# Kernel optimization log

Measured on AMD Instinct MI355X. Metric: run time of the kernel, lower is better.

## Reference

```python
import jax, jax.numpy as jnp
import numpy as np

# Grid config (matches init_kwargs): xbound/ybound [-50,50,0.5], zbound [-10,10,20]
NX = (200, 200, 1)                       # voxels per axis
DX = jnp.array([0.5, 0.5, 20.0], jnp.float32)      # voxel size
LO = jnp.array([-50.0, -50.0, -10.0], jnp.float32)  # grid lower corner (= bx - dx/2)
EXTENT = jnp.array([100.0, 100.0, 20.0], jnp.float32)

B, N, C, D, H, W = 2, 6, 64, 41, 32, 88


def setup_inputs() -> dict:
    key = jax.random.key(0)
    k1, k2, k3 = jax.random.split(key, 3)
    feat = jax.random.normal(k1, (B, N, C, H, W), jnp.float32)
    depth_logits = jax.random.normal(k2, (B, N, D, H, W), jnp.float32)
    geom = jax.random.uniform(k3, (B, N, D, H, W, 3), jnp.float32)  # normalized frustum->ego coords
    return {"feat": feat, "depth_logits": depth_logits, "geom": geom}


def reference(feat, depth_logits, geom):
    # --- Lift: depth-probability-weighted outer product ---
    depth = jax.nn.softmax(depth_logits, axis=2)               # [B,N,D,H,W]
    volume = jnp.einsum('bndhw,bnchw->bndhwc', depth, feat)    # [B,N,D,H,W,C]
    pts = volume.reshape(-1, C)                                # [P, C], P = B*N*D*H*W

    # --- Geometry -> voxel indices (frustum points in ego frame) ---
    world = geom * EXTENT + LO                                 # map [0,1]^3 to grid extent
    vox = jnp.floor((world - LO) / DX).astype(jnp.int32)       # [B,N,D,H,W,3]
    vox = vox.reshape(-1, 3)
    ix, iy, iz = vox[:, 0], vox[:, 1], vox[:, 2]

    nx0, nx1, nx2 = NX
    valid = ((ix >= 0) & (ix < nx0) & (iy >= 0) & (iy < nx1)
             & (iz >= 0) & (iz < nx2))                          # [P]

    pts_per_batch = N * D * H * W
    batch_ix = jnp.repeat(jnp.arange(B, dtype=jnp.int32), pts_per_batch)

    n_vox = nx0 * nx1 * nx2
    seg = ((batch_ix * nx0 + ix) * nx1 + iy) * nx2 + iz
    seg = jnp.where(valid, seg, B * n_vox)                     # invalid -> dummy bucket

    # --- Splat: per-voxel sum (== QuickCumsum sorted-cumsum-diff) ---
    pooled = jax.ops.segment_sum(pts, seg, num_segments=B * n_vox + 1)
    pooled = pooled[:-1].reshape(B, nx0, nx1, nx2, C)          # drop dummy

    # [B, C, Z, X, Y] then collapse Z (=1) into channels -> BEV [B, C, X, Y]
    bev = jnp.transpose(pooled, (0, 4, 3, 1, 2)).reshape(B, C * nx2, nx0, nx1)
    return bev
```

## Files before the change

### kernel.cpp

```cpp
#include <hip/hip_runtime.h>
#include <math.h>
#include <stdint.h>

namespace {
constexpr int kB = 2, kN = 6, kC = 64, kD = 41, kH = 32, kW = 88;
constexpr int kHW = kH * kW;
constexpr int kBN = kB * kN;
constexpr int kNX = 200;
constexpr int kVox = kNX * kNX;
constexpr int kPts = kBN * kD * kHW;
constexpr int kRows4 = kB * kNX * 4;
constexpr int kCap4 = 1120;
constexpr int kOvfCap = 4096;

constexpr int kTiles = kBN * (kHW / 64);
constexpr int kFusedBlks = kTiles * 2;
}

#define FP_BARRIER(x) asm volatile("" : "+v"(x))

__device__ __forceinline__ uint32_t f2bf_rne(float f) {
  uint32_t u = __float_as_uint(f);
  return (u + 0x7FFFu + ((u >> 16) & 1u)) >> 16;
}

__global__ void __launch_bounds__(256) lss_zero(unsigned* __restrict__ cnt) {
  for (int i = threadIdx.x; i <= kRows4; i += 256) cnt[i] = 0u;
}

__global__ void __launch_bounds__(512) lss_fused(
    const float* __restrict__ feat, uint32_t* __restrict__ featT,
    const float* __restrict__ logits, const float* __restrict__ geom,
    unsigned* __restrict__ cnt, uint2* __restrict__ list,
    unsigned* __restrict__ ovf_cnt, uint4* __restrict__ ovf) {
  int blk = blockIdx.x;
  int tid = threadIdx.x;
  if (blk < kTiles) {
    __shared__ float t[64][65];
    int bn = blk / 44, hw0 = (blk % 44) * 64;
    const float* src = feat + (size_t)bn * kC * kHW;
    for (int idx = tid; idx < 64 * 64; idx += 512) {
      int c = idx >> 6, hw = idx & 63;
      t[hw][c] = src[(size_t)c * kHW + hw0 + hw];
    }
    __syncthreads();
    uint32_t* dst = featT + ((size_t)bn * kHW + hw0) * 32;
    for (int idx = tid; idx < 64 * 32; idx += 512) {
      int hw = idx >> 5, j = idx & 31;
      uint32_t lo = f2bf_rne(t[hw][2 * j]);
      uint32_t hi = f2bf_rne(t[hw][2 * j + 1]);
      dst[(size_t)hw * 32 + j] = lo | (hi << 16);
    }
  } else {
    __shared__ unsigned shist[kRows4];
    __shared__ unsigned sbase[kRows4];
    __shared__ float smax[8 * 64];
    __shared__ float ssum[8 * 64];
    int tb = blk - kTiles;
    int bn = tb / 44, hw0 = (tb % 44) * 64;
    int hwl = tid & 63, dg = tid >> 6;
    int hw = hw0 + hwl;
    int b = (bn >= kN) ? 1 : 0;
    int col = bn * kHW + hw;
    int d0 = (dg * kD) >> 3, d1 = ((dg + 1) * kD) >> 3;
    for (int r = tid; r < kRows4; r += 512) shist[r] = 0;
    float x[6];
    float m = -INFINITY;
#pragma unroll
    for (int k = 0; k < 6; ++k) {
      int d = d0 + k;
      if (d < d1) {
        x[k] = logits[(size_t)(bn * kD + d) * kHW + hw];
        m = fmaxf(m, x[k]);
      }
    }
    smax[dg * 64 + hwl] = m;
    __syncthreads();
    float M = smax[hwl];
#pragma unroll
    for (int gg = 1; gg < 8; ++gg) M = fmaxf(M, smax[gg * 64 + hwl]);
    float s = 0.0f;
#pragma unroll
    for (int k = 0; k < 6; ++k) {
      int d = d0 + k;
      if (d < d1) { x[k] = expf(x[k] - M); s += x[k]; }
    }
    ssum[dg * 64 + hwl] = s;
    __syncthreads();
    float S = ssum[hwl];
#pragma unroll
    for (int gg = 1; gg < 8; ++gg) S += ssum[gg * 64 + hwl];
    int vv[6];
#pragma unroll
    for (int k = 0; k < 6; ++k) {
      vv[k] = -1;
      int d = d0 + k;
      if (d < d1) {
        size_t g = ((size_t)(bn * kD + d) * kHW + hw) * 3;
        float gx = geom[g + 0];
        float gy = geom[g + 1];
        float gz = geom[g + 2];
        float px = __fmul_rn(gx, 100.0f); FP_BARRIER(px);
        float py = __fmul_rn(gy, 100.0f); FP_BARRIER(py);
        float pz = __fmul_rn(gz, 20.0f);  FP_BARRIER(pz);
        float wx = __fsub_rn(px, 50.0f);  FP_BARRIER(wx);
        float wy = __fsub_rn(py, 50.0f);  FP_BARRIER(wy);
        float wz = __fsub_rn(pz, 10.0f);  FP_BARRIER(wz);
        float tx = __fadd_rn(wx, 50.0f);  FP_BARRIER(tx);
        float ty = __fadd_rn(wy, 50.0f);  FP_BARRIER(ty);
        float tz = __fadd_rn(wz, 10.0f);  FP_BARRIER(tz);
        float qx = __fdiv_rn(tx, 0.5f);   FP_BARRIER(qx);
        float qy = __fdiv_rn(ty, 0.5f);   FP_BARRIER(qy);
        float qz = __fdiv_rn(tz, 20.0f);  FP_BARRIER(qz);
        int ix = (int)floorf(qx);
        int iy = (int)floorf(qy);
        int iz = (int)floorf(qz);
        if ((unsigned)ix < (unsigned)kNX && (unsigned)iy < (unsigned)kNX &&
            (unsigned)iz < 1u) {
          vv[k] = (ix << 8) | iy;
          atomicAdd(&shist[((b * kNX + ix) << 2) + iy / 50], 1u);
        }
      }
    }
    __syncthreads();
    for (int r = tid; r < kRows4; r += 512)
      if (shist[r]) sbase[r] = atomicAdd(&cnt[r], shist[r]);
    __syncthreads();
#pragma unroll
    for (int k = 0; k < 6; ++k) {
      if (vv[k] < 0) continue;
      int ix = vv[k] >> 8, iy = vv[k] & 255;
      int row4 = ((b * kNX + ix) << 2) + iy / 50;
      float wgt = x[k] / S;
      unsigned key = ((unsigned)iy << 16) | (unsigned)col;
      unsigned pos = atomicAdd(&sbase[row4], 1u);
      if (pos < (unsigned)kCap4) {
        list[(size_t)row4 * kCap4 + pos] =
            make_uint2(key, __float_as_uint(wgt));
      } else {
        unsigned o = atomicAdd(ovf_cnt, 1u);
        if (o < (unsigned)kOvfCap)
          ovf[o] = make_uint4((unsigned)row4, key, __float_as_uint(wgt), 0u);
      }
    }
  }
}

__global__ void __launch_bounds__(256) lss_rowgather(
    const unsigned* __restrict__ cnt, const uint2* __restrict__ list,
    const uint32_t* __restrict__ featT, float* __restrict__ out,
    const unsigned* __restrict__ ovf_cnt, const uint4* __restrict__ ovf) {
  __shared__ uint2 sl[kCap4];
  __shared__ float accT[50 * 67];
  __shared__ unsigned hist[64];
  __shared__ unsigned off[51];
  __shared__ unsigned curb[50];
  int tid = threadIdx.x;
  int r4 = blockIdx.x;
  int q = r4 & 3;
  int r = r4 >> 2;
  int b = r / kNX, ix = r - (r / kNX) * kNX;
  int iyb = q * 50;
  size_t s0 = (size_t)r4 * kCap4;
  unsigned n = cnt[r4];
  unsigned ns = min(n, (unsigned)kCap4);

  if (tid < 64) hist[tid] = 0;
  __syncthreads();
  for (unsigned k = tid; k < ns; k += 256)
    atomicAdd(&hist[(list[s0 + k].x >> 16) - iyb], 1u);
  __syncthreads();
  unsigned c0 = (tid < 64) ? hist[tid] : 0u;
  for (int o = 1; o < 64; o <<= 1) {
    unsigned xx = (tid < 64 && tid >= o) ? hist[tid - o] : 0u;
    __syncthreads();
    if (tid < 64) hist[tid] += xx;
    __syncthreads();
  }
  if (tid < 50) {
    unsigned st = hist[tid] - c0;
    off[tid] = st;
    curb[tid] = st;
  }
  if (tid == 0) off[50] = ns;
  __syncthreads();
  for (unsigned k = tid; k < ns; k += 256) {
    uint2 a = list[s0 + k];
    unsigned pos = atomicAdd(&curb[(a.x >> 16) - iyb], 1u);
    sl[pos] = a;
  }
  __syncthreads();
  int wv = tid >> 6, lane = tid & 63;
  int g = lane >> 4, sub = lane & 15;
  int ly0 = wv * 13, ly1 = min(ly0 + 13, 50);
  for (int ly = ly0; ly < ly1; ++ly) {
    unsigned k = off[ly], e = off[ly + 1];
    float a0 = 0, a1 = 0, a2 = 0, a3 = 0;
    unsigned kk = k + g;
    for (; kk + 4 < e; kk += 8) {
      uint2 ea = sl[kk];
      uint2 eb = sl[kk + 4];
      uint2 fa = ((const uint2*)(featT + ((size_t)(ea.x & 0xFFFFu) << 5)))[sub];
      uint2 fb = ((const uint2*)(featT + ((size_t)(eb.x & 0xFFFFu) << 5)))[sub];
      float wa = __uint_as_float(ea.y), wb = __uint_as_float(eb.y);
      a0 += wa * __uint_as_float(fa.x << 16);
      a1 += wa * __uint_as_float(fa.x & 0xFFFF0000u);
      a2 += wa * __uint_as_float(fa.y << 16);
      a3 += wa * __uint_as_float(fa.y & 0xFFFF0000u);
      a0 += wb * __uint_as_float(fb.x << 16);
      a1 += wb * __uint_as_float(fb.x & 0xFFFF0000u);
      a2 += wb * __uint_as_float(fb.y << 16);
      a3 += wb * __uint_as_float(fb.y & 0xFFFF0000u);
    }
    if (kk < e) {
      uint2 ea = sl[kk];
      uint2 fa = ((const uint2*)(featT + ((size_t)(ea.x & 0xFFFFu) << 5)))[sub];
      float wa = __uint_as_float(ea.y);
      a0 += wa * __uint_as_float(fa.x << 16);
      a1 += wa * __uint_as_float(fa.x & 0xFFFF0000u);
      a2 += wa * __uint_as_float(fa.y << 16);
      a3 += wa * __uint_as_float(fa.y & 0xFFFF0000u);
    }
    a0 += __shfl_xor(a0, 16); a0 += __shfl_xor(a0, 32);
    a1 += __shfl_xor(a1, 16); a1 += __shfl_xor(a1, 32);
    a2 += __shfl_xor(a2, 16); a2 += __shfl_xor(a2, 32);
    a3 += __shfl_xor(a3, 16); a3 += __shfl_xor(a3, 32);
    if (g == 0) {
      float* dst = &accT[ly * 67 + (sub << 2)];
      dst[0] = a0; dst[1] = a1; dst[2] = a2; dst[3] = a3;
    }
  }
  __syncthreads();
  unsigned ovfn = min(*ovf_cnt, (unsigned)kOvfCap);
  if (ovfn > 0) {
    for (unsigned k = tid; k < ovfn; k += 256) {
      uint4 a = ovf[k];
      if (a.x != (unsigned)r4) continue;
      int ly = (int)(a.y >> 16) - iyb;
      const uint32_t* fr = featT + ((size_t)(a.y & 0xFFFFu) << 5);
      float w = __uint_as_float(a.z);
      for (int c = 0; c < kC; ++c) {
        uint32_t u = fr[c >> 1];
        float f = __uint_as_float((c & 1) ? (u & 0xFFFF0000u) : (u << 16));
        atomicAdd(&accT[ly * 67 + c], w * f);
      }
    }
    __syncthreads();
  }
  float* op = out + (size_t)b * kC * kVox + (size_t)ix * kNX + iyb;
  for (int idx = tid; idx < kC * 50; idx += 256) {
    int c = idx / 50, iy = idx - c * 50;
    op[(size_t)c * kVox + iy] = accT[iy * 67 + c];
  }
}

extern "C" void kernel_launch(void* const* d_in, const int* in_sizes, int n_in,
                              void* d_out, int out_size, void* d_ws,
                              size_t ws_size, hipStream_t stream) {
  const float* feat = (const float*)d_in[0];
  const float* logits = (const float*)d_in[1];
  const float* geom = (const float*)d_in[2];
  float* out = (float*)d_out;

  char* w = (char*)d_ws;
  uint2* list = (uint2*)w;         w += (size_t)kRows4 * kCap4 * 8;
  uint32_t* featT = (uint32_t*)w;  w += (size_t)kBN * kHW * 32 * 4;
  uint4* ovf = (uint4*)w;          w += (size_t)kOvfCap * 16;
  unsigned* cnt = (unsigned*)w;    w += (size_t)kRows4 * 4;
  unsigned* ovf_cnt = cnt + kRows4;

  lss_zero<<<1, 256, 0, stream>>>(cnt);
  lss_fused<<<kFusedBlks, 512, 0, stream>>>(feat, featT, logits, geom, cnt,
                                            list, ovf_cnt, ovf);
  lss_rowgather<<<kRows4, 256, 0, stream>>>(cnt, list, featT, out, ovf_cnt,
                                            ovf);
}
```

Before: 64.94 us.

## Assign eight lanes per output cell in row gather, widen to 512 threads

The gather stage now gives each of the 50 output cells its own group of 8 threads. Each thread loads 16-byte feature chunks covering 8 channels, where before 4 sub-groups of 16 lanes handled a cell serially and needed a cross-lane shuffle reduction. The block grows to 512 threads and the loop is unrolled by 4 to keep more independent loads in flight. The trade-off is more registers per thread, 112 idle threads per block, and a workload that becomes uneven across cells when point counts differ.

```diff
diff --git a/kernel.cpp b/kernel.cpp
--- a/kernel.cpp
+++ b/kernel.cpp
@@ -146,12 +146,12 @@
   }
 }
 
-__global__ void __launch_bounds__(256) lss_rowgather(
+__global__ void __launch_bounds__(512) lss_rowgather(
     const unsigned* __restrict__ cnt, const uint2* __restrict__ list,
     const uint32_t* __restrict__ featT, float* __restrict__ out,
     const unsigned* __restrict__ ovf_cnt, const uint4* __restrict__ ovf) {
   __shared__ uint2 sl[kCap4];
-  __shared__ float accT[50 * 67];
+  __shared__ float accT[50 * 65];
   __shared__ unsigned hist[64];
   __shared__ unsigned off[51];
   __shared__ unsigned curb[50];
@@ -167,7 +167,7 @@
 
   if (tid < 64) hist[tid] = 0;
   __syncthreads();
-  for (unsigned k = tid; k < ns; k += 256)
+  for (unsigned k = tid; k < ns; k += 512)
     atomicAdd(&hist[(list[s0 + k].x >> 16) - iyb], 1u);
   __syncthreads();
   unsigned c0 = (tid < 64) ? hist[tid] : 0u;
@@ -184,73 +184,98 @@
   }
   if (tid == 0) off[50] = ns;
   __syncthreads();
-  for (unsigned k = tid; k < ns; k += 256) {
+  for (unsigned k = tid; k < ns; k += 512) {
     uint2 a = list[s0 + k];
     unsigned pos = atomicAdd(&curb[(a.x >> 16) - iyb], 1u);
     sl[pos] = a;
   }
   __syncthreads();
-  int wv = tid >> 6, lane = tid & 63;
-  int g = lane >> 4, sub = lane & 15;
-  int ly0 = wv * 13, ly1 = min(ly0 + 13, 50);
-  for (int ly = ly0; ly < ly1; ++ly) {
+  int ly = tid >> 3, sub = tid & 7;
+  if (ly < 50) {
     unsigned k = off[ly], e = off[ly + 1];
-    float a0 = 0, a1 = 0, a2 = 0, a3 = 0;
-    unsigned kk = k + g;
-    for (; kk + 4 < e; kk += 8) {
-      uint2 ea = sl[kk];
-      uint2 eb = sl[kk + 4];
-      uint2 fa = ((const uint2*)(featT + ((size_t)(ea.x & 0xFFFFu) << 5)))[sub];
-      uint2 fb = ((const uint2*)(featT + ((size_t)(eb.x & 0xFFFFu) << 5)))[sub];
-      float wa = __uint_as_float(ea.y), wb = __uint_as_float(eb.y);
-      a0 += wa * __uint_as_float(fa.x << 16);
-      a1 += wa * __uint_as_float(fa.x & 0xFFFF0000u);
-      a2 += wa * __uint_as_float(fa.y << 16);
-      a3 += wa * __uint_as_float(fa.y & 0xFFFF0000u);
-      a0 += wb * __uint_as_float(fb.x << 16);
-      a1 += wb * __uint_as_float(fb.x & 0xFFFF0000u);
-      a2 += wb * __uint_as_float(fb.y << 16);
-      a3 += wb * __uint_as_float(fb.y & 0xFFFF0000u);
-    }
-    if (kk < e) {
-      uint2 ea = sl[kk];
-      uint2 fa = ((const uint2*)(featT + ((size_t)(ea.x & 0xFFFFu) << 5)))[sub];
+    float a0 = 0, a1 = 0, a2 = 0, a3 = 0, a4 = 0, a5 = 0, a6 = 0, a7 = 0;
+    for (; k + 4 <= e; k += 4) {
+      uint2 e0 = sl[k + 0];
+      uint2 e1 = sl[k + 1];
+      uint2 e2 = sl[k + 2];
+      uint2 e3 = sl[k + 3];
+      uint4 f0 = ((const uint4*)(featT + ((size_t)(e0.x & 0xFFFFu) << 5)))[sub];
+      uint4 f1 = ((const uint4*)(featT + ((size_t)(e1.x & 0xFFFFu) << 5)))[sub];
+      uint4 f2 = ((const uint4*)(featT + ((size_t)(e2.x & 0xFFFFu) << 5)))[sub];
+      uint4 f3 = ((const uint4*)(featT + ((size_t)(e3.x & 0xFFFFu) << 5)))[sub];
+      float w0 = __uint_as_float(e0.y), w1 = __uint_as_float(e1.y);
+      float w2 = __uint_as_float(e2.y), w3 = __uint_as_float(e3.y);
+      a0 += w0 * __uint_as_float(f0.x << 16);
+      a1 += w0 * __uint_as_float(f0.x & 0xFFFF0000u);
+      a2 += w0 * __uint_as_float(f0.y << 16);
+      a3 += w0 * __uint_as_float(f0.y & 0xFFFF0000u);
+      a4 += w0 * __uint_as_float(f0.z << 16);
+      a5 += w0 * __uint_as_float(f0.z & 0xFFFF0000u);
+      a6 += w0 * __uint_as_float(f0.w << 16);
+      a7 += w0 * __uint_as_float(f0.w & 0xFFFF0000u);
+      a0 += w1 * __uint_as_float(f1.x << 16);
+      a1 += w1 * __uint_as_float(f1.x & 0xFFFF0000u);
+      a2 += w1 * __uint_as_float(f1.y << 16);
+      a3 += w1 * __uint_as_float(f1.y & 0xFFFF0000u);
+      a4 += w1 * __uint_as_float(f1.z << 16);
+      a5 += w1 * __uint_as_float(f1.z & 0xFFFF0000u);
+      a6 += w1 * __uint_as_float(f1.w << 16);
+      a7 += w1 * __uint_as_float(f1.w & 0xFFFF0000u);
+      a0 += w2 * __uint_as_float(f2.x << 16);
+      a1 += w2 * __uint_as_float(f2.x & 0xFFFF0000u);
+      a2 += w2 * __uint_as_float(f2.y << 16);
+      a3 += w2 * __uint_as_float(f2.y & 0xFFFF0000u);
+      a4 += w2 * __uint_as_float(f2.z << 16);
+      a5 += w2 * __uint_as_float(f2.z & 0xFFFF0000u);
+      a6 += w2 * __uint_as_float(f2.w << 16);
+      a7 += w2 * __uint_as_float(f2.w & 0xFFFF0000u);
+      a0 += w3 * __uint_as_float(f3.x << 16);
+      a1 += w3 * __uint_as_float(f3.x & 0xFFFF0000u);
+      a2 += w3 * __uint_as_float(f3.y << 16);
+      a3 += w3 * __uint_as_float(f3.y & 0xFFFF0000u);
+      a4 += w3 * __uint_as_float(f3.z << 16);
+      a5 += w3 * __uint_as_float(f3.z & 0xFFFF0000u);
+      a6 += w3 * __uint_as_float(f3.w << 16);
+      a7 += w3 * __uint_as_float(f3.w & 0xFFFF0000u);
+    }
+    for (; k < e; ++k) {
+      uint2 ea = sl[k];
+      uint4 fa = ((const uint4*)(featT + ((size_t)(ea.x & 0xFFFFu) << 5)))[sub];
       float wa = __uint_as_float(ea.y);
       a0 += wa * __uint_as_float(fa.x << 16);
       a1 += wa * __uint_as_float(fa.x & 0xFFFF0000u);
       a2 += wa * __uint_as_float(fa.y << 16);
       a3 += wa * __uint_as_float(fa.y & 0xFFFF0000u);
-    }
-    a0 += __shfl_xor(a0, 16); a0 += __shfl_xor(a0, 32);
-    a1 += __shfl_xor(a1, 16); a1 += __shfl_xor(a1, 32);
-    a2 += __shfl_xor(a2, 16); a2 += __shfl_xor(a2, 32);
-    a3 += __shfl_xor(a3, 16); a3 += __shfl_xor(a3, 32);
-    if (g == 0) {
-      float* dst = &accT[ly * 67 + (sub << 2)];
-      dst[0] = a0; dst[1] = a1; dst[2] = a2; dst[3] = a3;
-    }
+      a4 += wa * __uint_as_float(fa.z << 16);
+      a5 += wa * __uint_as_float(fa.z & 0xFFFF0000u);
+      a6 += wa * __uint_as_float(fa.w << 16);
+      a7 += wa * __uint_as_float(fa.w & 0xFFFF0000u);
+    }
+    float* dst = &accT[ly * 65 + (sub << 3)];
+    dst[0] = a0; dst[1] = a1; dst[2] = a2; dst[3] = a3;
+    dst[4] = a4; dst[5] = a5; dst[6] = a6; dst[7] = a7;
   }
   __syncthreads();
   unsigned ovfn = min(*ovf_cnt, (unsigned)kOvfCap);
   if (ovfn > 0) {
-    for (unsigned k = tid; k < ovfn; k += 256) {
+    for (unsigned k = tid; k < ovfn; k += 512) {
       uint4 a = ovf[k];
       if (a.x != (unsigned)r4) continue;
-      int ly = (int)(a.y >> 16) - iyb;
+      int lyo = (int)(a.y >> 16) - iyb;
       const uint32_t* fr = featT + ((size_t)(a.y & 0xFFFFu) << 5);
       float w = __uint_as_float(a.z);
       for (int c = 0; c < kC; ++c) {
         uint32_t u = fr[c >> 1];
         float f = __uint_as_float((c & 1) ? (u & 0xFFFF0000u) : (u << 16));
-        atomicAdd(&accT[ly * 67 + c], w * f);
+        atomicAdd(&accT[lyo * 65 + c], w * f);
       }
     }
     __syncthreads();
   }
   float* op = out + (size_t)b * kC * kVox + (size_t)ix * kNX + iyb;
-  for (int idx = tid; idx < kC * 50; idx += 256) {
+  for (int idx = tid; idx < kC * 50; idx += 512) {
     int c = idx / 50, iy = idx - c * 50;
-    op[(size_t)c * kVox + iy] = accT[iy * 67 + c];
+    op[(size_t)c * kVox + iy] = accT[iy * 65 + c];
   }
 }
 
@@ -272,6 +297,6 @@
   lss_zero<<<1, 256, 0, stream>>>(cnt);
   lss_fused<<<kFusedBlks, 512, 0, stream>>>(feat, featT, logits, geom, cnt,
                                             list, ovf_cnt, ovf);
-  lss_rowgather<<<kRows4, 256, 0, stream>>>(cnt, list, featT, out, ovf_cnt,
+  lss_rowgather<<<kRows4, 512, 0, stream>>>(cnt, list, featT, out, ovf_cnt,
                                             ovf);
 }
```

After: 56.20 us. 13.5% less time.

## Widen rowgather blocks to 512 threads with register-held entries and wave scan

Applied to the files above, without the earlier changes.

The row-gather kernel now runs 512 threads per block, and each thread loads up to three list entries once into registers, so the histogram and scatter passes share a single global read. The multi-barrier shared-memory prefix scan becomes a single-wave shuffle scan. Rows are assigned to waves round-robin, with deeper 4-way unrolled gathers. Block IDs are swizzled across 8 groups, and the accT stride changes to 68. The changes aim to cut global reloads, barriers and per-row latency, at the cost of more registers per thread and a stride change whose bank-conflict effect is unclear.

```diff
diff --git a/kernel.cpp b/kernel.cpp
--- a/kernel.cpp
+++ b/kernel.cpp
@@ -22,6 +22,13 @@
 __device__ __forceinline__ uint32_t f2bf_rne(float f) {
   uint32_t u = __float_as_uint(f);
   return (u + 0x7FFFu + ((u >> 16) & 1u)) >> 16;
+}
+
+__device__ __forceinline__ float bf_lo(uint32_t u) {
+  return __uint_as_float(u << 16);
+}
+__device__ __forceinline__ float bf_hi(uint32_t u) {
+  return __uint_as_float(u & 0xFFFF0000u);
 }
 
 __global__ void __launch_bounds__(256) lss_zero(unsigned* __restrict__ cnt) {
@@ -146,17 +153,17 @@
   }
 }
 
-__global__ void __launch_bounds__(256) lss_rowgather(
+__global__ void __launch_bounds__(512) lss_rowgather(
     const unsigned* __restrict__ cnt, const uint2* __restrict__ list,
     const uint32_t* __restrict__ featT, float* __restrict__ out,
     const unsigned* __restrict__ ovf_cnt, const uint4* __restrict__ ovf) {
   __shared__ uint2 sl[kCap4];
-  __shared__ float accT[50 * 67];
+  __shared__ float accT[50 * 68];
   __shared__ unsigned hist[64];
   __shared__ unsigned off[51];
   __shared__ unsigned curb[50];
   int tid = threadIdx.x;
-  int r4 = blockIdx.x;
+  int r4 = ((blockIdx.x & 7) * (kRows4 / 8)) + (blockIdx.x >> 3);
   int q = r4 & 3;
   int r = r4 >> 2;
   int b = r / kNX, ix = r - (r / kNX) * kNX;
@@ -167,90 +174,99 @@
 
   if (tid < 64) hist[tid] = 0;
   __syncthreads();
-  for (unsigned k = tid; k < ns; k += 256)
-    atomicAdd(&hist[(list[s0 + k].x >> 16) - iyb], 1u);
-  __syncthreads();
-  unsigned c0 = (tid < 64) ? hist[tid] : 0u;
-  for (int o = 1; o < 64; o <<= 1) {
-    unsigned xx = (tid < 64 && tid >= o) ? hist[tid - o] : 0u;
-    __syncthreads();
-    if (tid < 64) hist[tid] += xx;
-    __syncthreads();
-  }
-  if (tid < 50) {
-    unsigned st = hist[tid] - c0;
-    off[tid] = st;
-    curb[tid] = st;
-  }
-  if (tid == 0) off[50] = ns;
-  __syncthreads();
-  for (unsigned k = tid; k < ns; k += 256) {
-    uint2 a = list[s0 + k];
-    unsigned pos = atomicAdd(&curb[(a.x >> 16) - iyb], 1u);
-    sl[pos] = a;
-  }
+  uint2 e0, e1, e2;
+  unsigned k0 = tid, k1 = tid + 512, k2 = tid + 1024;
+  if (k0 < ns) { e0 = list[s0 + k0]; atomicAdd(&hist[(e0.x >> 16) - iyb], 1u); }
+  if (k1 < ns) { e1 = list[s0 + k1]; atomicAdd(&hist[(e1.x >> 16) - iyb], 1u); }
+  if (k2 < ns) { e2 = list[s0 + k2]; atomicAdd(&hist[(e2.x >> 16) - iyb], 1u); }
+  __syncthreads();
+  if (tid < 64) {
+    unsigned v = hist[tid];
+    unsigned sc = v;
+#pragma unroll
+    for (int o = 1; o < 64; o <<= 1) {
+      unsigned y = __shfl_up(sc, o);
+      if (tid >= o) sc += y;
+    }
+    if (tid < 50) {
+      off[tid] = sc - v;
+      curb[tid] = sc - v;
+    }
+    if (tid == 0) off[50] = ns;
+  }
+  __syncthreads();
+  if (k0 < ns) sl[atomicAdd(&curb[(e0.x >> 16) - iyb], 1u)] = e0;
+  if (k1 < ns) sl[atomicAdd(&curb[(e1.x >> 16) - iyb], 1u)] = e1;
+  if (k2 < ns) sl[atomicAdd(&curb[(e2.x >> 16) - iyb], 1u)] = e2;
   __syncthreads();
   int wv = tid >> 6, lane = tid & 63;
-  int g = lane >> 4, sub = lane & 15;
-  int ly0 = wv * 13, ly1 = min(ly0 + 13, 50);
-  for (int ly = ly0; ly < ly1; ++ly) {
-    unsigned k = off[ly], e = off[ly + 1];
+  int ep = lane >> 4;
+  int cu = (lane & 15) * 2;
+  for (int ly = wv; ly < 50; ly += 8) {
+    unsigned kk = off[ly], e = off[ly + 1];
     float a0 = 0, a1 = 0, a2 = 0, a3 = 0;
-    unsigned kk = k + g;
-    for (; kk + 4 < e; kk += 8) {
-      uint2 ea = sl[kk];
-      uint2 eb = sl[kk + 4];
-      uint2 fa = ((const uint2*)(featT + ((size_t)(ea.x & 0xFFFFu) << 5)))[sub];
-      uint2 fb = ((const uint2*)(featT + ((size_t)(eb.x & 0xFFFFu) << 5)))[sub];
-      float wa = __uint_as_float(ea.y), wb = __uint_as_float(eb.y);
-      a0 += wa * __uint_as_float(fa.x << 16);
-      a1 += wa * __uint_as_float(fa.x & 0xFFFF0000u);
-      a2 += wa * __uint_as_float(fa.y << 16);
-      a3 += wa * __uint_as_float(fa.y & 0xFFFF0000u);
-      a0 += wb * __uint_as_float(fb.x << 16);
-      a1 += wb * __uint_as_float(fb.x & 0xFFFF0000u);
-      a2 += wb * __uint_as_float(fb.y << 16);
-      a3 += wb * __uint_as_float(fb.y & 0xFFFF0000u);
-    }
-    if (kk < e) {
-      uint2 ea = sl[kk];
-      uint2 fa = ((const uint2*)(featT + ((size_t)(ea.x & 0xFFFFu) << 5)))[sub];
-      float wa = __uint_as_float(ea.y);
-      a0 += wa * __uint_as_float(fa.x << 16);
-      a1 += wa * __uint_as_float(fa.x & 0xFFFF0000u);
-      a2 += wa * __uint_as_float(fa.y << 16);
-      a3 += wa * __uint_as_float(fa.y & 0xFFFF0000u);
+    for (; kk + 16 <= e; kk += 16) {
+      unsigned k = kk + ep;
+      uint2 x0 = sl[k];
+      uint2 x1 = sl[k + 4];
+      uint2 x2 = sl[k + 8];
+      uint2 x3 = sl[k + 12];
+      uint2 f0 = *(const uint2*)(featT + ((size_t)(x0.x & 0xFFFFu) << 5) + cu);
+      uint2 f1 = *(const uint2*)(featT + ((size_t)(x1.x & 0xFFFFu) << 5) + cu);
+      uint2 f2 = *(const uint2*)(featT + ((size_t)(x2.x & 0xFFFFu) << 5) + cu);
+      uint2 f3 = *(const uint2*)(featT + ((size_t)(x3.x & 0xFFFFu) << 5) + cu);
+      float w0 = __uint_as_float(x0.y), w1 = __uint_as_float(x1.y);
+      float w2 = __uint_as_float(x2.y), w3 = __uint_as_float(x3.y);
+      a0 += w0 * bf_lo(f0.x); a1 += w0 * bf_hi(f0.x);
+      a2 += w0 * bf_lo(f0.y); a3 += w0 * bf_hi(f0.y);
+      a0 += w1 * bf_lo(f1.x); a1 += w1 * bf_hi(f1.x);
+      a2 += w1 * bf_lo(f1.y); a3 += w1 * bf_hi(f1.y);
+      a0 += w2 * bf_lo(f2.x); a1 += w2 * bf_hi(f2.x);
+      a2 += w2 * bf_lo(f2.y); a3 += w2 * bf_hi(f2.y);
+      a0 += w3 * bf_lo(f3.x); a1 += w3 * bf_hi(f3.x);
+      a2 += w3 * bf_lo(f3.y); a3 += w3 * bf_hi(f3.y);
+    }
+    for (; kk < e; kk += 4) {
+      unsigned k = kk + ep;
+      if (k < e) {
+        uint2 x0 = sl[k];
+        uint2 f0 =
+            *(const uint2*)(featT + ((size_t)(x0.x & 0xFFFFu) << 5) + cu);
+        float w0 = __uint_as_float(x0.y);
+        a0 += w0 * bf_lo(f0.x); a1 += w0 * bf_hi(f0.x);
+        a2 += w0 * bf_lo(f0.y); a3 += w0 * bf_hi(f0.y);
+      }
     }
     a0 += __shfl_xor(a0, 16); a0 += __shfl_xor(a0, 32);
     a1 += __shfl_xor(a1, 16); a1 += __shfl_xor(a1, 32);
     a2 += __shfl_xor(a2, 16); a2 += __shfl_xor(a2, 32);
     a3 += __shfl_xor(a3, 16); a3 += __shfl_xor(a3, 32);
-    if (g == 0) {
-      float* dst = &accT[ly * 67 + (sub << 2)];
+    if (ep == 0) {
+      float* dst = &accT[ly * 68 + (lane & 15) * 4];
       dst[0] = a0; dst[1] = a1; dst[2] = a2; dst[3] = a3;
     }
   }
   __syncthreads();
   unsigned ovfn = min(*ovf_cnt, (unsigned)kOvfCap);
   if (ovfn > 0) {
-    for (unsigned k = tid; k < ovfn; k += 256) {
+    for (unsigned k = tid; k < ovfn; k += 512) {
       uint4 a = ovf[k];
       if (a.x != (unsigned)r4) continue;
-      int ly = (int)(a.y >> 16) - iyb;
+      int lyo = (int)(a.y >> 16) - iyb;
       const uint32_t* fr = featT + ((size_t)(a.y & 0xFFFFu) << 5);
       float w = __uint_as_float(a.z);
       for (int c = 0; c < kC; ++c) {
         uint32_t u = fr[c >> 1];
-        float f = __uint_as_float((c & 1) ? (u & 0xFFFF0000u) : (u << 16));
-        atomicAdd(&accT[ly * 67 + c], w * f);
+        float f = (c & 1) ? bf_hi(u) : bf_lo(u);
+        atomicAdd(&accT[lyo * 68 + c], w * f);
       }
     }
     __syncthreads();
   }
   float* op = out + (size_t)b * kC * kVox + (size_t)ix * kNX + iyb;
-  for (int idx = tid; idx < kC * 50; idx += 256) {
+  for (int idx = tid; idx < kC * 50; idx += 512) {
     int c = idx / 50, iy = idx - c * 50;
-    op[(size_t)c * kVox + iy] = accT[iy * 67 + c];
+    op[(size_t)c * kVox + iy] = accT[iy * 68 + c];
   }
 }
 
@@ -272,6 +288,6 @@
   lss_zero<<<1, 256, 0, stream>>>(cnt);
   lss_fused<<<kFusedBlks, 512, 0, stream>>>(feat, featT, logits, geom, cnt,
                                             list, ovf_cnt, ovf);
-  lss_rowgather<<<kRows4, 256, 0, stream>>>(cnt, list, featT, out, ovf_cnt,
+  lss_rowgather<<<kRows4, 512, 0, stream>>>(cnt, list, featT, out, ovf_cnt,
                                             ovf);
 }
```

Result: faster. 61.35 us (-5.5%).
